# Kernel optimization log

Measured on AMD Instinct MI355X. Metric: run time of the kernel, lower is better.

Reference implementation:

```python
import jax, jax.numpy as jnp
import numpy as np

NQ, NK = 32, 128  # local window sizes from AttentionIndex defaults
N_HEADS = 8


def _build_index(M):
    """Precompute block-sparse local attention indices (static, numpy).
    Returns query_idx [C,NQ], query_mask [C,NQ], key_idx [C,NK], key_mask [C,NK].
    """
    C = (M + NQ - 1) // NQ
    half = (NQ - 1.0) * 0.5
    centers = np.round(np.arange(half, M + half, NQ, dtype=np.float32)).astype(np.int64)
    q_idx = np.arange(C * NQ, dtype=np.int64)
    q_mask = q_idx < M
    q_idx = np.where(q_mask, q_idx, 0).reshape(C, NQ)
    q_mask = q_mask.reshape(C, NQ)
    key_idx = np.zeros((C, NK), np.int64)
    key_mask = np.zeros((C, NK), bool)
    for i, c in enumerate(centers):
        s = max(int(c) - NK // 2, 0)
        e = min(int(c) + NK // 2, M)
        w = e - s
        key_idx[i, :w] = np.arange(s, e, dtype=np.int64)
        key_mask[i, :w] = True
    return (jnp.asarray(q_idx), jnp.asarray(q_mask),
            jnp.asarray(key_idx), jnp.asarray(key_mask))


def setup_inputs() -> dict:
    key = jax.random.key(0)
    ks = jax.random.split(key, 6)
    B, M, D, N = 2, 16384, 256, 2048
    f_atom = jax.random.normal(ks[0], (B, M, D), jnp.float32)
    atom_mask = jnp.ones((B, M), jnp.float32)
    atom_token_uid = jnp.sort(jax.random.randint(ks[1], (B, M), 0, N), axis=-1)
    scale = 1.0 / np.sqrt(D)
    Wq = jax.random.normal(ks[2], (D, D), jnp.float32) * scale
    Wk = jax.random.normal(ks[3], (D, D), jnp.float32) * scale
    Wv = jax.random.normal(ks[4], (D, D), jnp.float32) * scale
    Wo = jax.random.normal(ks[5], (D, D), jnp.float32) * scale
    return {"f_atom": f_atom, "atom_mask": atom_mask, "Wq": Wq, "Wk": Wk,
            "Wv": Wv, "Wo": Wo, "atom_token_uid": atom_token_uid, "n_token": N}


def reference(f_atom, atom_mask, Wq, Wk, Wv, Wo, atom_token_uid, n_token):
    B, M, D = f_atom.shape
    H = N_HEADS
    dh = D // H
    q_idx, q_mask, k_idx, k_mask = _build_index(M)
    C = q_idx.shape[0]

    # projections -> [B,M,H,dh]
    q = (f_atom @ Wq).reshape(B, M, H, dh)
    k = (f_atom @ Wk).reshape(B, M, H, dh)
    v = (f_atom @ Wv).reshape(B, M, H, dh)

    # gather into local windows: queries [B,C,NQ,H,dh], keys/values [B,C,NK,H,dh]
    qb = q[:, q_idx]
    kb = k[:, k_idx]
    vb = v[:, k_idx]

    key_valid = (atom_mask[:, k_idx] > 0) & k_mask[None]            # [B,C,NK]
    alpha_mask = q_mask[None, None, :, :, None] & key_valid[:, None, :, None, :]  # [B,H,C,NQ,NK] (bcast)

    scores = jnp.einsum('bcqhd,bckhd->bhcqk', qb, kb) / np.sqrt(dh)  # [B,H,C,NQ,NK]
    scores = jnp.where(alpha_mask, scores, jnp.float32(-1e9))
    attn = jax.nn.softmax(scores, axis=-1)

    out = jnp.einsum('bhcqk,bckhd->bcqhd', attn, vb)                 # [B,C,NQ,H,dh]
    out = out.reshape(B, C * NQ, D)[:, :M] @ Wo                      # scatter back to [B,M,D]
    out = out * atom_mask[..., None]

    # aggregate atom feats -> token feats (masked segment mean), pad to n_token
    def agg(data, seg, mask):
        s = jax.ops.segment_sum(data * mask[:, None], seg, num_segments=n_token)
        cnt = jax.ops.segment_sum(mask, seg, num_segments=n_token)
        return s / (cnt[:, None] + 1e-8)

    f_token = jax.vmap(agg)(out, atom_token_uid, atom_mask)          # [B,N,D]
    return f_token
```

## Files before the change

### kernel.cpp

```cpp
#include <hip/hip_runtime.h>

typedef _Float16 f16;
typedef _Float16 f16x4 __attribute__((ext_vector_type(4)));
typedef _Float16 f16x8 __attribute__((ext_vector_type(8)));
typedef float    f32x16 __attribute__((ext_vector_type(16)));

#define MFMA(a, b, c) __builtin_amdgcn_mfma_f32_32x32x16_f16((a), (b), (c), 0, 0, 0)

static constexpr int Mg   = 16384;
static constexpr int Bg   = 2;
static constexpr int Dg   = 256;
static constexpr int Hg   = 8;
static constexpr int Cg   = 512;
static constexpr int Ntok = 2048;
static constexpr float QSCALE = 0.17677669529663687f;

typedef __attribute__((address_space(1))) const void gbl_cv;
typedef __attribute__((address_space(3))) void lds_v;

static __device__ __forceinline__ void gll16(const f16* g, f16* l) {
    __builtin_amdgcn_global_load_lds((gbl_cv*)g, (lds_v*)l, 16, 0, 0);
}
static __device__ __forceinline__ f16x8 mk8(f16x4 a, f16x4 b) {
    f16x8 r;
    r[0] = a[0]; r[1] = a[1]; r[2] = a[2]; r[3] = a[3];
    r[4] = b[0]; r[5] = b[1]; r[6] = b[2]; r[7] = b[3];
    return r;
}

__global__ __launch_bounds__(256) void k_wt(const float* __restrict__ Wq,
                                            const float* __restrict__ Wk,
                                            const float* __restrict__ Wv,
                                            const float* __restrict__ Wo,
                                            f16* __restrict__ Wsw) {
    int idx = blockIdx.x * 256 + threadIdx.x;
    int w   = idx >> 16;
    int rem = idx & 65535;
    int k   = rem >> 8;
    int n   = rem & 255;
    if (w < 3) {
        const float* W = (w == 0) ? Wq : (w == 1) ? Wk : Wv;
        int G = (k >> 3) ^ (n & 7);
        Wsw[w * 65536 + n * 256 + (G << 3) + (k & 7)] = (f16)W[k * 256 + n];
    } else {
        Wsw[3 * 65536 + ((k >> 3) * 256 + n) * 8 + (k & 7)] = (f16)Wo[k * 256 + n];
    }
}

__global__ __launch_bounds__(256, 2) void k_qkv(const float* __restrict__ A,
                                                const f16* __restrict__ Wsw,
                                                f16* __restrict__ Qo,
                                                f16* __restrict__ Ko,
                                                f16* __restrict__ VW) {
    __shared__ f16 Ls[2][32 * 256];

    const int tid  = threadIdx.x;
    const int d    = blockIdx.x;
    const int lin  = (d & 7) * 64 + (d >> 3);
    const int yt   = lin >> 1;
    const int half = lin & 1;
    const int m0   = yt * 128;
    const int lane = tid & 63, w = tid >> 6;
    const int l31  = lane & 31, hi = lane >> 5;
    const int mrow = m0 + 32 * w + l31;
    const int xr   = l31 & 7;

    f16x8 a[16];
    const float* ap = A + (size_t)mrow * 256 + 8 * hi;
#pragma unroll
    for (int g = 0; g < 16; ++g) {
        float4 v0 = *reinterpret_cast<const float4*>(ap + 16 * g);
        float4 v1 = *reinterpret_cast<const float4*>(ap + 16 * g + 4);
        f16x8 t;
        t[0] = (f16)v0.x; t[1] = (f16)v0.y; t[2] = (f16)v0.z; t[3] = (f16)v0.w;
        t[4] = (f16)v1.x; t[5] = (f16)v1.y; t[6] = (f16)v1.z; t[7] = (f16)v1.w;
        a[g] = t;
    }

#define STW(S, BB)                                                             \
    {                                                                          \
        const f16* src = Wsw + ((S) >> 3) * 65536 + (((S) & 7) * 32) * 256;    \
        _Pragma("unroll")                                                      \
        for (int i = 0; i < 4; ++i) {                                          \
            int g2 = i * 256 + tid;                                            \
            gll16(src + g2 * 8, &Ls[BB][g2 * 8]);                              \
        }                                                                      \
    }

#define QKV_STEP(S, BB)                                                        \
    {                                                                          \
        if ((S) + 1 < s_end) { STW((S) + 1, (BB) ^ 1); }                       \
        f32x16 acc;                                                            \
        _Pragma("unroll")                                                      \
        for (int e = 0; e < 16; ++e) acc[e] = 0.f;                             \
        _Pragma("unroll")                                                      \
        for (int g = 0; g < 16; ++g) {                                         \
            f16x8 bf = *(const f16x8*)&Ls[BB][l31 * 256 +                      \
                                             (((2 * g + hi) ^ xr) << 3)];      \
            acc = MFMA(a[g], bf, acc);                                         \
        }                                                                      \
        const int wix  = (S) >> 3;                                             \
        const int gcol = ((S) & 7) * 32 + l31;                                 \
        const int mb   = m0 + 32 * w + 4 * hi;                                 \
        if (wix == 0) {                                                        \
            _Pragma("unroll")                                                  \
            for (int r = 0; r < 16; ++r)                                       \
                Qo[(size_t)(mb + (r & 3) + 8 * (r >> 2)) * 256 + gcol] =       \
                    (f16)(acc[r] * QSCALE);                                    \
        } else if (wix == 1) {                                                 \
            _Pragma("unroll")                                                  \
            for (int r = 0; r < 16; ++r)                                       \
                Ko[(size_t)(mb + (r & 3) + 8 * (r >> 2)) * 256 + gcol] =       \
                    (f16)acc[r];                                               \
        } else {                                                               \
            _Pragma("unroll")                                                  \
            for (int rq = 0; rq < 4; ++rq) {                                   \
                f16x4 pv = { (f16)acc[rq * 4 + 0], (f16)acc[rq * 4 + 1],       \
                             (f16)acc[rq * 4 + 2], (f16)acc[rq * 4 + 3] };     \
                int mr  = mb + 8 * rq;                                         \
                int bb2 = mr >> 14;                                            \
                int msg = (mr & 16383) >> 3;                                   \
                *reinterpret_cast<f16x4*>(VW + ((size_t)(bb2 * 2048 + msg) *   \
                                          256 + gcol) * 8 + 4 * hi) = pv;      \
            }                                                                  \
        }                                                                      \
        if ((S) + 1 < s_end) {                                                 \
            if (((S) >> 3) == 2) {                                             \
                asm volatile("s_waitcnt vmcnt(4)" ::: "memory");               \
            } else {                                                           \
                asm volatile("s_waitcnt vmcnt(16)" ::: "memory");              \
            }                                                                  \
            __builtin_amdgcn_s_barrier();                                      \
            __builtin_amdgcn_sched_barrier(0);                                 \
        }                                                                      \
    }

#define QKV_RUN(BASE)                                                          \
    {                                                                          \
        const int s_end = (BASE) + 12;                                         \
        STW(BASE, 0);                                                          \
        asm volatile("s_waitcnt vmcnt(0)" ::: "memory");                       \
        __builtin_amdgcn_s_barrier();                                          \
        __builtin_amdgcn_sched_barrier(0);                                     \
        _Pragma("unroll")                                                      \
        for (int ss = 0; ss < 12; ++ss) { QKV_STEP((BASE) + ss, ss & 1); }     \
    }

    if (half == 0) { QKV_RUN(0); } else { QKV_RUN(12); }
#undef QKV_RUN
#undef QKV_STEP
#undef STW
}

__global__ __launch_bounds__(512, 2) void k_attn(const f16* __restrict__ Qo,
                                                 const f16* __restrict__ Ko,
                                                 const f16* __restrict__ VW,
                                                 const f16* __restrict__ Wsw,
                                                 f16* __restrict__ OUT) {
    __shared__ f16 Ks[128 * 256];
    __shared__ f16 Qs[32 * 256];

    const int tid  = threadIdx.x;
    const int idx  = blockIdx.x;
    const int lin  = (idx & 7) * 128 + (idx >> 3);
    const int b    = lin >> 9;
    const int c    = lin & 511;
    const int h    = tid >> 6;
    const int l31  = tid & 31;
    const int hi   = (tid & 63) >> 5;

    const int u0 = 32 * c - 48;
    const int e0 = (32 * c + 80 < Mg) ? (32 * c + 80) : Mg;

    const f16* Kb = Ko + (size_t)b * Mg * 256;
#pragma unroll
    for (int i = 0; i < 8; ++i) {
        int g = i * 512 + tid;
        int r = g >> 5, s = g & 31;
        int m = u0 + r;
        m = m < 0 ? 0 : (m > Mg - 1 ? Mg - 1 : m);
        gll16(Kb + (size_t)m * 256 + ((s ^ (r & 31)) << 3), &Ks[g * 8]);
    }
    const f16* Qb = Qo + ((size_t)b * Mg + 32 * c) * 256;
#pragma unroll
    for (int i = 0; i < 2; ++i) {
        int g = i * 512 + tid;
        int r = g >> 5, s = g & 31;
        gll16(Qb + (size_t)r * 256 + ((s ^ r) << 3), &Qs[g * 8]);
    }
    __syncthreads();

    f16x8 qf0 = *(const f16x8*)&Qs[l31 * 256 + (((4 * h + hi) ^ l31) << 3)];
    f16x8 qf1 = *(const f16x8*)&Qs[l31 * 256 + (((4 * h + 2 + hi) ^ l31) << 3)];

    f32x16 p4[4];
#pragma unroll
    for (int t = 0; t < 4; ++t)
#pragma unroll
        for (int e = 0; e < 16; ++e) p4[t][e] = 0.f;

#pragma unroll
    for (int t = 0; t < 4; ++t) {
        int rr = 32 * t + l31;
        f16x8 kf0 = *(const f16x8*)&Ks[rr * 256 + (((4 * h + hi) ^ l31) << 3)];
        f16x8 kf1 = *(const f16x8*)&Ks[rr * 256 + (((4 * h + 2 + hi) ^ l31) << 3)];
        p4[t] = MFMA(kf0, qf0, p4[t]);
        p4[t] = MFMA(kf1, qf1, p4[t]);
    }

    const f16* Vbb = VW + (size_t)b * 2048 * 256 * 8;
    f16x4 v0r[8], v1r[8];
#pragma unroll
    for (int s = 0; s < 8; ++s) {
        int g0 = (u0 >> 3) + 2 * s;
        int g1 = g0 + 1;
        g0 = g0 < 0 ? 0 : (g0 > 2047 ? 2047 : g0);
        g1 = g1 < 0 ? 0 : (g1 > 2047 ? 2047 : g1);
        v0r[s] = *(const f16x4*)(Vbb + ((size_t)g0 * 256 + 32 * h + l31) * 8 + 4 * hi);
        v1r[s] = *(const f16x4*)(Vbb + ((size_t)g1 * 256 + 32 * h + l31) * 8 + 4 * hi);
    }

    float mx = -3e38f;
#pragma unroll
    for (int t = 0; t < 4; ++t)
#pragma unroll
        for (int r = 0; r < 16; ++r) {
            int gm = u0 + 32 * t + (r & 3) + 8 * (r >> 2) + 4 * hi;
            if (gm >= 0 && gm < e0) mx = fmaxf(mx, p4[t][r]);
        }
    mx = fmaxf(mx, __shfl_xor(mx, 32));

    float sum = 0.f;
#pragma unroll
    for (int t = 0; t < 4; ++t)
#pragma unroll
        for (int r = 0; r < 16; ++r) {
            int gm = u0 + 32 * t + (r & 3) + 8 * (r >> 2) + 4 * hi;
            float ev = (gm >= 0 && gm < e0) ? __expf(p4[t][r] - mx) : 0.f;
            p4[t][r] = ev;
            sum += ev;
        }
    sum += __shfl_xor(sum, 32);
    const float inv = 1.f / sum;
#pragma unroll
    for (int t = 0; t < 4; ++t)
#pragma unroll
        for (int e = 0; e < 16; ++e) p4[t][e] *= inv;

    f32x16 o;
#pragma unroll
    for (int e = 0; e < 16; ++e) o[e] = 0.f;

#pragma unroll
    for (int s = 0; s < 8; ++s) {
        f16x8 pa;
#pragma unroll
        for (int e = 0; e < 8; ++e) pa[e] = (f16)(p4[s >> 1][8 * (s & 1) + e]);
        o = MFMA(pa, mk8(v0r[s], v1r[s]), o);
    }

    __syncthreads();
    {
        const int col = h * 32 + l31;
#pragma unroll
        for (int r = 0; r < 16; ++r) {
            int row = (r & 3) + 8 * (r >> 2) + 4 * hi;
            Ks[row * 264 + col] = (f16)o[r];
        }
    }
    __syncthreads();

    {
        const f16* Wb = Wsw + 3 * 65536;
        f32x16 acc;
#pragma unroll
        for (int e = 0; e < 16; ++e) acc[e] = 0.f;
#pragma unroll
        for (int g = 0; g < 16; ++g) {
            int gp = 2 * g + hi;
            f16x8 av = *(const f16x8*)&Ks[l31 * 264 + gp * 8];
            f16x8 bv = *(const f16x8*)(Wb + ((size_t)gp * 256 + 32 * h + l31) * 8);
            acc = MFMA(av, bv, acc);
        }
#pragma unroll
        for (int r = 0; r < 16; ++r) {
            int row = (r & 3) + 8 * (r >> 2) + 4 * hi;
            OUT[((size_t)b * Mg + 32 * c + row) * 256 + h * 32 + l31] = (f16)acc[r];
        }
    }
}

__global__ __launch_bounds__(256) void k_seg(const f16* __restrict__ OUT,
                                             const int* __restrict__ uid,
                                             const float* __restrict__ mask,
                                             float* __restrict__ out) {
    const int t = blockIdx.x, b = blockIdx.y;
    const int d = threadIdx.x;
    const int* u = uid + b * Mg;

    int lo = 0, hi = Mg;
    while (lo < hi) { int mid = (lo + hi) >> 1; if (u[mid] < t) lo = mid + 1; else hi = mid; }
    int lo2 = lo, hi2 = Mg;
    while (lo2 < hi2) { int mid = (lo2 + hi2) >> 1; if (u[mid] < t + 1) lo2 = mid + 1; else hi2 = mid; }

    float sum = 0.f, cnt = 0.f;
    for (int m = lo; m < lo2; ++m) {
        float msk = mask[b * Mg + m];
        sum += msk * msk * (float)OUT[((size_t)b * Mg + m) * 256 + d];
        cnt += msk;
    }
    out[((size_t)b * Ntok + t) * 256 + d] = sum / (cnt + 1e-8f);
}

extern "C" void kernel_launch(void* const* d_in, const int* in_sizes, int n_in,
                              void* d_out, int out_size, void* d_ws, size_t ws_size,
                              hipStream_t stream) {
    const float* f_atom = (const float*)d_in[0];
    const float* amask  = (const float*)d_in[1];
    const float* Wq     = (const float*)d_in[2];
    const float* Wk     = (const float*)d_in[3];
    const float* Wv     = (const float*)d_in[4];
    const float* Wo     = (const float*)d_in[5];
    const int*   uid    = (const int*)d_in[6];

    const size_t HALF_WT  = 4 * 65536;
    const size_t HALF_MAT = (size_t)Bg * Mg * Dg;
    const size_t needed_bytes = (HALF_WT + 4 * HALF_MAT) * sizeof(f16);
    if (ws_size < needed_bytes) return;

    f16* Wsw  = (f16*)d_ws;
    f16* Qb   = Wsw + HALF_WT;
    f16* Kb   = Qb + HALF_MAT;
    f16* VWb  = Kb + HALF_MAT;
    f16* OUTb = VWb + HALF_MAT;

    k_wt  <<<dim3(1024), 256, 0, stream>>>(Wq, Wk, Wv, Wo, Wsw);
    k_qkv <<<dim3(512), 256, 0, stream>>>(f_atom, Wsw, Qb, Kb, VWb);
    k_attn<<<dim3(1024), 512, 0, stream>>>(Qb, Kb, VWb, Wsw, OUTb);
    k_seg <<<dim3(Ntok, Bg), 256, 0, stream>>>(OUTb, uid, amask, (float*)d_out);
}
```

Baseline: 78.72 us.

## Precompute segment starts, overlap loads, fast-path unmasked softmax, raise MFMA priority

Moves the per-token binary searches out of the segment kernel into the weight-prep kernel, which now writes a table of segment start offsets that k_seg reads. In k_qkv the first weight tile is issued before the activations are loaded, so the two transfers overlap. In k_attn the V register loads are issued before the QK MFMAs, and a separate softmax path without index masking is used for windows that lie fully inside the sequence. The MFMA regions are also wrapped in s_setprio. These changes add code paths and slightly more workspace, and the priority hints may or may not help scheduling.

```diff
diff --git a/kernel.cpp b/kernel.cpp
--- a/kernel.cpp
+++ b/kernel.cpp
@@ -32,7 +32,9 @@
                                             const float* __restrict__ Wk,
                                             const float* __restrict__ Wv,
                                             const float* __restrict__ Wo,
-                                            f16* __restrict__ Wsw) {
+                                            const int* __restrict__ uid,
+                                            f16* __restrict__ Wsw,
+                                            int* __restrict__ starts) {
     int idx = blockIdx.x * 256 + threadIdx.x;
     int w   = idx >> 16;
     int rem = idx & 65535;
@@ -45,6 +47,13 @@
     } else {
         Wsw[3 * 65536 + ((k >> 3) * 256 + n) * 8 + (k & 7)] = (f16)Wo[k * 256 + n];
     }
+    if (idx < 2 * 2049) {
+        int b = idx / 2049, t = idx % 2049;
+        const int* u = uid + b * Mg;
+        int lo = 0, hi = Mg;
+        while (lo < hi) { int mid = (lo + hi) >> 1; if (u[mid] < t) lo = mid + 1; else hi = mid; }
+        starts[idx] = lo;
+    }
 }
 
 __global__ __launch_bounds__(256, 2) void k_qkv(const float* __restrict__ A,
@@ -65,18 +74,6 @@
     const int mrow = m0 + 32 * w + l31;
     const int xr   = l31 & 7;
 
-    f16x8 a[16];
-    const float* ap = A + (size_t)mrow * 256 + 8 * hi;
-#pragma unroll
-    for (int g = 0; g < 16; ++g) {
-        float4 v0 = *reinterpret_cast<const float4*>(ap + 16 * g);
-        float4 v1 = *reinterpret_cast<const float4*>(ap + 16 * g + 4);
-        f16x8 t;
-        t[0] = (f16)v0.x; t[1] = (f16)v0.y; t[2] = (f16)v0.z; t[3] = (f16)v0.w;
-        t[4] = (f16)v1.x; t[5] = (f16)v1.y; t[6] = (f16)v1.z; t[7] = (f16)v1.w;
-        a[g] = t;
-    }
-
 #define STW(S, BB)                                                             \
     {                                                                          \
         const f16* src = Wsw + ((S) >> 3) * 65536 + (((S) & 7) * 32) * 256;    \
@@ -85,6 +82,20 @@
             int g2 = i * 256 + tid;                                            \
             gll16(src + g2 * 8, &Ls[BB][g2 * 8]);                              \
         }                                                                      \
+    }
+
+    if (half == 0) { STW(0, 0); } else { STW(12, 0); }
+
+    f16x8 a[16];
+    const float* ap = A + (size_t)mrow * 256 + 8 * hi;
+#pragma unroll
+    for (int g = 0; g < 16; ++g) {
+        float4 v0 = *reinterpret_cast<const float4*>(ap + 16 * g);
+        float4 v1 = *reinterpret_cast<const float4*>(ap + 16 * g + 4);
+        f16x8 t;
+        t[0] = (f16)v0.x; t[1] = (f16)v0.y; t[2] = (f16)v0.z; t[3] = (f16)v0.w;
+        t[4] = (f16)v1.x; t[5] = (f16)v1.y; t[6] = (f16)v1.z; t[7] = (f16)v1.w;
+        a[g] = t;
     }
 
 #define QKV_STEP(S, BB)                                                        \
@@ -138,7 +149,6 @@
 #define QKV_RUN(BASE)                                                          \
     {                                                                          \
         const int s_end = (BASE) + 12;                                         \
-        STW(BASE, 0);                                                          \
         asm volatile("s_waitcnt vmcnt(0)" ::: "memory");                       \
         __builtin_amdgcn_s_barrier();                                          \
         __builtin_amdgcn_sched_barrier(0);                                     \
@@ -171,6 +181,7 @@
 
     const int u0 = 32 * c - 48;
     const int e0 = (32 * c + 80 < Mg) ? (32 * c + 80) : Mg;
+    const bool full = (u0 >= 0) && (32 * c + 80 <= Mg);
 
     const f16* Kb = Ko + (size_t)b * Mg * 256;
 #pragma unroll
@@ -189,24 +200,6 @@
         gll16(Qb + (size_t)r * 256 + ((s ^ r) << 3), &Qs[g * 8]);
     }
     __syncthreads();
-
-    f16x8 qf0 = *(const f16x8*)&Qs[l31 * 256 + (((4 * h + hi) ^ l31) << 3)];
-    f16x8 qf1 = *(const f16x8*)&Qs[l31 * 256 + (((4 * h + 2 + hi) ^ l31) << 3)];
-
-    f32x16 p4[4];
-#pragma unroll
-    for (int t = 0; t < 4; ++t)
-#pragma unroll
-        for (int e = 0; e < 16; ++e) p4[t][e] = 0.f;
-
-#pragma unroll
-    for (int t = 0; t < 4; ++t) {
-        int rr = 32 * t + l31;
-        f16x8 kf0 = *(const f16x8*)&Ks[rr * 256 + (((4 * h + hi) ^ l31) << 3)];
-        f16x8 kf1 = *(const f16x8*)&Ks[rr * 256 + (((4 * h + 2 + hi) ^ l31) << 3)];
-        p4[t] = MFMA(kf0, qf0, p4[t]);
-        p4[t] = MFMA(kf1, qf1, p4[t]);
-    }
 
     const f16* Vbb = VW + (size_t)b * 2048 * 256 * 8;
     f16x4 v0r[8], v1r[8];
@@ -220,26 +213,61 @@
         v1r[s] = *(const f16x4*)(Vbb + ((size_t)g1 * 256 + 32 * h + l31) * 8 + 4 * hi);
     }
 
+    f16x8 qf0 = *(const f16x8*)&Qs[l31 * 256 + (((4 * h + hi) ^ l31) << 3)];
+    f16x8 qf1 = *(const f16x8*)&Qs[l31 * 256 + (((4 * h + 2 + hi) ^ l31) << 3)];
+
+    f32x16 p4[4];
+#pragma unroll
+    for (int t = 0; t < 4; ++t)
+#pragma unroll
+        for (int e = 0; e < 16; ++e) p4[t][e] = 0.f;
+
+    __builtin_amdgcn_s_setprio(1);
+#pragma unroll
+    for (int t = 0; t < 4; ++t) {
+        int rr = 32 * t + l31;
+        f16x8 kf0 = *(const f16x8*)&Ks[rr * 256 + (((4 * h + hi) ^ l31) << 3)];
+        f16x8 kf1 = *(const f16x8*)&Ks[rr * 256 + (((4 * h + 2 + hi) ^ l31) << 3)];
+        p4[t] = MFMA(kf0, qf0, p4[t]);
+        p4[t] = MFMA(kf1, qf1, p4[t]);
+    }
+    __builtin_amdgcn_s_setprio(0);
+
     float mx = -3e38f;
-#pragma unroll
-    for (int t = 0; t < 4; ++t)
-#pragma unroll
-        for (int r = 0; r < 16; ++r) {
-            int gm = u0 + 32 * t + (r & 3) + 8 * (r >> 2) + 4 * hi;
-            if (gm >= 0 && gm < e0) mx = fmaxf(mx, p4[t][r]);
-        }
-    mx = fmaxf(mx, __shfl_xor(mx, 32));
-
     float sum = 0.f;
-#pragma unroll
-    for (int t = 0; t < 4; ++t)
-#pragma unroll
-        for (int r = 0; r < 16; ++r) {
-            int gm = u0 + 32 * t + (r & 3) + 8 * (r >> 2) + 4 * hi;
-            float ev = (gm >= 0 && gm < e0) ? __expf(p4[t][r] - mx) : 0.f;
-            p4[t][r] = ev;
-            sum += ev;
-        }
+    if (full) {
+#pragma unroll
+        for (int t = 0; t < 4; ++t)
+#pragma unroll
+            for (int r = 0; r < 16; ++r) mx = fmaxf(mx, p4[t][r]);
+        mx = fmaxf(mx, __shfl_xor(mx, 32));
+#pragma unroll
+        for (int t = 0; t < 4; ++t)
+#pragma unroll
+            for (int r = 0; r < 16; ++r) {
+                float ev = __expf(p4[t][r] - mx);
+                p4[t][r] = ev;
+                sum += ev;
+            }
+    } else {
+#pragma unroll
+        for (int t = 0; t < 4; ++t)
+#pragma unroll
+            for (int r = 0; r < 16; ++r) {
+                int gm = u0 + 32 * t + (r & 3) + 8 * (r >> 2) + 4 * hi;
+                if (gm >= 0 && gm < e0) mx = fmaxf(mx, p4[t][r]);
+            }
+        mx = fmaxf(mx, __shfl_xor(mx, 32));
+#pragma unroll
+        for (int t = 0; t < 4; ++t)
+#pragma unroll
+            for (int r = 0; r < 16; ++r) {
+                int gm = u0 + 32 * t + (r & 3) + 8 * (r >> 2) + 4 * hi;
+                float ev = (gm >= 0 && gm < e0) ? __expf(p4[t][r] - mx) : 0.f;
+                p4[t][r] = ev;
+                sum += ev;
+            }
+    }
     sum += __shfl_xor(sum, 32);
     const float inv = 1.f / sum;
 #pragma unroll
@@ -247,10 +275,14 @@
 #pragma unroll
         for (int e = 0; e < 16; ++e) p4[t][e] *= inv;
 
+    asm volatile("s_waitcnt vmcnt(0)" ::: "memory");
+    __builtin_amdgcn_sched_barrier(0);
+
     f32x16 o;
 #pragma unroll
     for (int e = 0; e < 16; ++e) o[e] = 0.f;
 
+    __builtin_amdgcn_s_setprio(1);
 #pragma unroll
     for (int s = 0; s < 8; ++s) {
         f16x8 pa;
@@ -258,6 +290,7 @@
         for (int e = 0; e < 8; ++e) pa[e] = (f16)(p4[s >> 1][8 * (s & 1) + e]);
         o = MFMA(pa, mk8(v0r[s], v1r[s]), o);
     }
+    __builtin_amdgcn_s_setprio(0);
 
     __syncthreads();
     {
@@ -275,6 +308,7 @@
         f32x16 acc;
 #pragma unroll
         for (int e = 0; e < 16; ++e) acc[e] = 0.f;
+        __builtin_amdgcn_s_setprio(1);
 #pragma unroll
         for (int g = 0; g < 16; ++g) {
             int gp = 2 * g + hi;
@@ -282,6 +316,7 @@
             f16x8 bv = *(const f16x8*)(Wb + ((size_t)gp * 256 + 32 * h + l31) * 8);
             acc = MFMA(av, bv, acc);
         }
+        __builtin_amdgcn_s_setprio(0);
 #pragma unroll
         for (int r = 0; r < 16; ++r) {
             int row = (r & 3) + 8 * (r >> 2) + 4 * hi;
@@ -291,17 +326,14 @@
 }
 
 __global__ __launch_bounds__(256) void k_seg(const f16* __restrict__ OUT,
-                                             const int* __restrict__ uid,
+                                             const int* __restrict__ starts,
                                              const float* __restrict__ mask,
                                              float* __restrict__ out) {
     const int t = blockIdx.x, b = blockIdx.y;
     const int d = threadIdx.x;
-    const int* u = uid + b * Mg;
-
-    int lo = 0, hi = Mg;
-    while (lo < hi) { int mid = (lo + hi) >> 1; if (u[mid] < t) lo = mid + 1; else hi = mid; }
-    int lo2 = lo, hi2 = Mg;
-    while (lo2 < hi2) { int mid = (lo2 + hi2) >> 1; if (u[mid] < t + 1) lo2 = mid + 1; else hi2 = mid; }
+
+    const int lo  = starts[b * 2049 + t];
+    const int lo2 = starts[b * 2049 + t + 1];
 
     float sum = 0.f, cnt = 0.f;
     for (int m = lo; m < lo2; ++m) {
@@ -325,7 +357,7 @@
 
     const size_t HALF_WT  = 4 * 65536;
     const size_t HALF_MAT = (size_t)Bg * Mg * Dg;
-    const size_t needed_bytes = (HALF_WT + 4 * HALF_MAT) * sizeof(f16);
+    const size_t needed_bytes = (HALF_WT + 4 * HALF_MAT) * sizeof(f16) + 2 * 2049 * sizeof(int);
     if (ws_size < needed_bytes) return;
 
     f16* Wsw  = (f16*)d_ws;
@@ -333,9 +365,10 @@
     f16* Kb   = Qb + HALF_MAT;
     f16* VWb  = Kb + HALF_MAT;
     f16* OUTb = VWb + HALF_MAT;
-
-    k_wt  <<<dim3(1024), 256, 0, stream>>>(Wq, Wk, Wv, Wo, Wsw);
+    int* starts = (int*)(OUTb + HALF_MAT);
+
+    k_wt  <<<dim3(1024), 256, 0, stream>>>(Wq, Wk, Wv, Wo, uid, Wsw, starts);
     k_qkv <<<dim3(512), 256, 0, stream>>>(f_atom, Wsw, Qb, Kb, VWb);
     k_attn<<<dim3(1024), 512, 0, stream>>>(Qb, Kb, VWb, Wsw, OUTb);
-    k_seg <<<dim3(Ntok, Bg), 256, 0, stream>>>(OUTb, uid, amask, (float*)d_out);
-}
+    k_seg <<<dim3(Ntok, Bg), 256, 0, stream>>>(OUTb, starts, amask, (float*)d_out);
+}
```

After: 73.00 us. 7.3% less time.
